# Performance work log

Measured on AMD Instinct MI355X. Metric: run time of the kernel, lower is better.

## Reference

```python
import jax, jax.numpy as jnp
import numpy as np

# tree structure: B trees, layer sizes per tree 2048 -> 256 -> 32 -> 1 (arities 8, 8, 32)
B = 256
N0, N1, N2, N3 = B * 2048, B * 256, B * 32, B * 1
D_IN, HID, OUT = 128, 256, 10
EPS = 1e-5


def _bn(x, g, b):
    # BatchNorm1d, training-mode batch stats (biased variance), as in torch
    mu = jnp.mean(x, axis=0)
    var = jnp.var(x, axis=0)
    return (x - mu) * jax.lax.rsqrt(var + EPS) * g + b


def _tree_layer(pooled, w1, b1, bn1g, bn1b, w2, b2, bng, bnb):
    # MLP(2 layers): Linear -> BN -> ReLU -> Linear, then outer BN -> ReLU (next_layer)
    z = jax.nn.relu(_bn(pooled @ w1 + b1, bn1g, bn1b))
    z = z @ w2 + b2
    return jax.nn.relu(_bn(z, bng, bnb))


def setup_inputs() -> dict:
    key = jax.random.key(0)
    ks = jax.random.split(key, 12)
    s = 0.05
    ar = lambda n: jnp.arange(n, dtype=jnp.int32)
    inp = {
        'x': jax.random.normal(ks[0], (N0, D_IN), jnp.float32),
        # child -> parent index (global, trees are contiguous blocks)
        'parent1': ar(N0) // 8,
        'parent2': ar(N1) // 8,
        'parent3': ar(N2) // 32,
        # node -> tree id per layer (for sum tree-pooling readout)
        'tree0': ar(N0) // 2048,
        'tree1': ar(N1) // 256,
        'tree2': ar(N2) // 32,
        # layer 1 MLP (input_dim -> hidden)
        'l1_w1': jax.random.normal(ks[1], (D_IN, HID), jnp.float32) * s,
        'l1_b1': jnp.zeros((HID,), jnp.float32),
        'l1_bn1g': jnp.ones((HID,), jnp.float32),
        'l1_bn1b': jnp.zeros((HID,), jnp.float32),
        'l1_w2': jax.random.normal(ks[2], (HID, HID), jnp.float32) * s,
        'l1_b2': jnp.zeros((HID,), jnp.float32),
        'l1_bng': jnp.ones((HID,), jnp.float32),
        'l1_bnb': jnp.zeros((HID,), jnp.float32),
        # layers 2 and 3 MLPs (hidden -> hidden), stacked on axis 0
        'lw1': jax.random.normal(ks[3], (2, HID, HID), jnp.float32) * s,
        'lb1': jnp.zeros((2, HID), jnp.float32),
        'lbn1g': jnp.ones((2, HID), jnp.float32),
        'lbn1b': jnp.zeros((2, HID), jnp.float32),
        'lw2': jax.random.normal(ks[4], (2, HID, HID), jnp.float32) * s,
        'lb2': jnp.zeros((2, HID), jnp.float32),
        'lbng': jnp.ones((2, HID), jnp.float32),
        'lbnb': jnp.zeros((2, HID), jnp.float32),
        # prediction heads
        'pred0_w': jax.random.normal(ks[5], (D_IN, OUT), jnp.float32) * s,
        'pred0_b': jnp.zeros((OUT,), jnp.float32),
        'predh_w': jax.random.normal(ks[6], (3, HID, OUT), jnp.float32) * s,
        'predh_b': jnp.zeros((3, OUT), jnp.float32),
    }
    return inp


def reference(x, parent1, parent2, parent3, tree0, tree1, tree2,
              l1_w1, l1_b1, l1_bn1g, l1_bn1b, l1_w2, l1_b2, l1_bng, l1_bnb,
              lw1, lb1, lbn1g, lbn1b, lw2, lb2, lbng, lbnb,
              pred0_w, pred0_b, predh_w, predh_b):
    seg = jax.ops.segment_sum
    h0 = x
    # layer 1: sparse child pooling (spmm == segment_sum) + MLP + BN + ReLU
    h1 = _tree_layer(seg(h0, parent1, num_segments=N1),
                     l1_w1, l1_b1, l1_bn1g, l1_bn1b, l1_w2, l1_b2, l1_bng, l1_bnb)
    h2 = _tree_layer(seg(h1, parent2, num_segments=N2),
                     lw1[0], lb1[0], lbn1g[0], lbn1b[0], lw2[0], lb2[0], lbng[0], lbnb[0])
    h3 = _tree_layer(seg(h2, parent3, num_segments=N3),
                     lw1[1], lb1[1], lbn1g[1], lbn1b[1], lw2[1], lb2[1], lbng[1], lbnb[1])
    # sum tree-pooling readout over layers 0..depth-1, plus root-layer linear
    score = seg(h0, tree0, num_segments=B) @ pred0_w + pred0_b
    score = score + seg(h1, tree1, num_segments=B) @ predh_w[0] + predh_b[0]
    score = score + seg(h2, tree2, num_segments=B) @ predh_w[1] + predh_b[1]
    score = score + h3 @ predh_w[2] + predh_b[2]  # h3 has 1 root per tree -> [B, OUT]
    return score
```

## Files before the change

### kernel.cpp

```cpp
#include <hip/hip_runtime.h>
#include <hip/hip_bf16.h>


#define N0 (256*2048)
#define N1 (256*256)
#define N2 (256*32)
#define NB 256
#define BN_EPS 1e-5f
#define NSLOT 8

typedef __attribute__((ext_vector_type(8))) __bf16 bf16x8;
typedef __attribute__((ext_vector_type(8))) unsigned short u16x8;
typedef __attribute__((ext_vector_type(4))) unsigned short u16x4;
typedef __attribute__((ext_vector_type(4))) float f32x4;

__device__ inline float bf2f(unsigned short b) {
    unsigned u = ((unsigned)b) << 16;
    float f; __builtin_memcpy(&f, &u, 4); return f;
}
__device__ inline unsigned short f2bf(float f) {
    unsigned u; __builtin_memcpy(&u, &f, 4);
    u += 0x7fff + ((u >> 16) & 1);
    return (unsigned short)(u >> 16);
}

__global__ __launch_bounds__(256) void prep_weights(const float* __restrict__ l1_w1,
                                                    const float* __restrict__ l1_w2,
                                                    const float* __restrict__ lw1,
                                                    const float* __restrict__ lw2,
                                                    unsigned short* __restrict__ Wt) {
    int idx = blockIdx.x * 256 + threadIdx.x;
    if (idx >= 360448) return;
    float v;
    if (idx < 32768) {
        int n = idx >> 7, k = idx & 127;
        v = l1_w1[k * 256 + n];
    } else if (idx < 98304) {
        int j = idx - 32768, n = j >> 8, k = j & 255;
        v = l1_w2[k * 256 + n];
    } else if (idx < 163840) {
        int j = idx - 98304, n = j >> 8, k = j & 255;
        v = lw1[k * 256 + n];
    } else if (idx < 229376) {
        int j = idx - 163840, n = j >> 8, k = j & 255;
        v = lw2[k * 256 + n];
    } else if (idx < 294912) {
        int j = idx - 229376, n = j >> 8, k = j & 255;
        v = lw1[65536 + k * 256 + n];
    } else {
        int j = idx - 294912, n = j >> 8, k = j & 255;
        v = lw2[65536 + k * 256 + n];
    }
    Wt[idx] = f2bf(v);
}

__device__ inline void bn_prologue(int tid, const float* __restrict__ partials,
                                   const float* __restrict__ g, const float* __restrict__ b,
                                   float invM, float* sc_lds, float* sh_lds) {
    if (tid < 256) {
        float s = 0.f, s2 = 0.f;
#pragma unroll
        for (int k = 0; k < NSLOT; ++k) {
            s  += partials[k * 512 + tid];
            s2 += partials[k * 512 + 256 + tid];
        }
        float mean = s * invM;
        float var = s2 * invM - mean * mean;
        float sc = g[tid] * rsqrtf(var + BN_EPS);
        sc_lds[tid] = sc;
        sh_lds[tid] = b[tid] - mean * sc;
    }
}

__global__ __launch_bounds__(512) void gemm1_fused(const float* __restrict__ x,
                                                   const unsigned short* __restrict__ Wt,
                                                   const float* __restrict__ bias,
                                                   unsigned short* __restrict__ Z1,
                                                   float* __restrict__ stat_partials,
                                                   float* __restrict__ ts0) {
    constexpr int LDA = 136, LDB = 72;
    __shared__ unsigned short Asb[128 * LDA];
    __shared__ unsigned short Bsb[256 * LDB];
    const int tid = threadIdx.x;
    const int c4 = tid & 31, rg = tid >> 5;
    const int m0 = blockIdx.x * 128;
    const int tree = blockIdx.x >> 1;
    f32x4 colp = {0.f, 0.f, 0.f, 0.f};
#pragma unroll
    for (int i = 0; i < 8; ++i) {
        int row = rg * 8 + i;
        const f32x4* xp = reinterpret_cast<const f32x4*>(x + (size_t)(m0 + row) * 1024 + c4 * 4);
        f32x4 s = {0.f, 0.f, 0.f, 0.f};
#pragma unroll
        for (int c = 0; c < 8; ++c) s += xp[c * 32];
        u16x4 o;
#pragma unroll
        for (int e = 0; e < 4; ++e) o[e] = f2bf(s[e]);
        *reinterpret_cast<u16x4*>(&Asb[row * LDA + c4 * 4]) = o;
        colp += s;
    }
#pragma unroll
    for (int e = 0; e < 4; ++e) atomicAdd(&ts0[tree * 128 + c4 * 4 + e], colp[e]);

    const int wave = tid >> 6, lane = tid & 63;
    const int q = lane >> 4, r = lane & 15;
    const int wc = wave & 3, wr = wave >> 2;
    f32x4 acc[4][4];
#pragma unroll
    for (int i = 0; i < 4; ++i)
#pragma unroll
        for (int j = 0; j < 4; ++j) acc[i][j] = (f32x4){0.f, 0.f, 0.f, 0.f};

#pragma unroll
    for (int s2 = 0; s2 < 2; ++s2) {
#pragma unroll
        for (int i = 0; i < 4; ++i) {
            int v = tid + i * 512;
            int n = v >> 3, kc = v & 7;
            u16x8 d = *reinterpret_cast<const u16x8*>(Wt + (size_t)n * 128 + s2 * 64 + kc * 8);
            *reinterpret_cast<u16x8*>(&Bsb[n * LDB + kc * 8]) = d;
        }
        __syncthreads();
#pragma unroll
        for (int s = 0; s < 2; ++s) {
            bf16x8 a[4], b[4];
#pragma unroll
            for (int i = 0; i < 4; ++i)
                a[i] = *reinterpret_cast<const bf16x8*>(&Asb[(wr * 64 + i * 16 + r) * LDA + s2 * 64 + s * 32 + q * 8]);
#pragma unroll
            for (int j = 0; j < 4; ++j)
                b[j] = *reinterpret_cast<const bf16x8*>(&Bsb[(wc * 64 + j * 16 + r) * LDB + s * 32 + q * 8]);
#pragma unroll
            for (int i = 0; i < 4; ++i)
#pragma unroll
                for (int j = 0; j < 4; ++j)
                    acc[i][j] = __builtin_amdgcn_mfma_f32_16x16x32_bf16(a[i], b[j], acc[i][j], 0, 0, 0);
        }
        __syncthreads();
    }
    float sj[4], s2j[4];
#pragma unroll
    for (int j = 0; j < 4; ++j) {
        float bj = bias[wc * 64 + j * 16 + r];
        float s = 0.f, s2 = 0.f;
#pragma unroll
        for (int i = 0; i < 4; ++i)
#pragma unroll
            for (int e = 0; e < 4; ++e) {
                acc[i][j][e] += bj;
                float v = acc[i][j][e];
                s += v; s2 += v * v;
            }
        s  += __shfl_xor(s, 16);  s  += __shfl_xor(s, 32);
        s2 += __shfl_xor(s2, 16); s2 += __shfl_xor(s2, 32);
        sj[j] = s; s2j[j] = s2;
    }
#pragma unroll
    for (int i = 0; i < 4; ++i)
#pragma unroll
        for (int e = 0; e < 4; ++e) {
            size_t row = m0 + wr * 64 + i * 16 + q * 4 + e;
#pragma unroll
            for (int j = 0; j < 4; ++j)
                Z1[row * 256 + wc * 64 + j * 16 + r] = f2bf(acc[i][j][e]);
        }
    if (q == 0) {
        int slot = blockIdx.x & (NSLOT - 1);
#pragma unroll
        for (int j = 0; j < 4; ++j) {
            int col = wc * 64 + j * 16 + r;
            atomicAdd(&stat_partials[slot * 512 + col], sj[j]);
            atomicAdd(&stat_partials[slot * 512 + 256 + col], s2j[j]);
        }
    }
}

__global__ __launch_bounds__(256) void gemm2_fused(const unsigned short* __restrict__ Z2,
                                                   const float* __restrict__ partials_in,
                                                   const float* __restrict__ bn_g,
                                                   const float* __restrict__ bn_b,
                                                   float invM,
                                                   const unsigned short* __restrict__ Wt2,
                                                   const float* __restrict__ bias,
                                                   unsigned short* __restrict__ Z2a,
                                                   float* __restrict__ stat_partials,
                                                   float* __restrict__ ts1) {
    constexpr int LDA = 264, LDB = 72;
    __shared__ unsigned short Asb[64 * LDA];
    __shared__ unsigned short Bsb[256 * LDB];
    __shared__ float sc_lds[256], sh_lds[256];
    const int tid = threadIdx.x;
    bn_prologue(tid, partials_in, bn_g, bn_b, invM, sc_lds, sh_lds);
    __syncthreads();
    const int c8 = tid & 31, rg = tid >> 5;
    const int m0 = blockIdx.x * 64;
    const int d0 = c8 * 8;
    float sc[8], sh[8], colp[8];
#pragma unroll
    for (int e = 0; e < 8; ++e) { sc[e] = sc_lds[d0 + e]; sh[e] = sh_lds[d0 + e]; colp[e] = 0.f; }
#pragma unroll
    for (int i = 0; i < 8; ++i) {
        int row = rg * 8 + i;
        float s[8];
#pragma unroll
        for (int e = 0; e < 8; ++e) s[e] = 0.f;
#pragma unroll
        for (int c = 0; c < 8; ++c) {
            u16x8 z = *reinterpret_cast<const u16x8*>(Z2 + ((size_t)(m0 + row) * 8 + c) * 256 + d0);
#pragma unroll
            for (int e = 0; e < 8; ++e) {
                float f = sc[e] * bf2f(z[e]) + sh[e];
                s[e] += f > 0.f ? f : 0.f;
            }
        }
        u16x8 o;
#pragma unroll
        for (int e = 0; e < 8; ++e) { o[e] = f2bf(s[e]); colp[e] += s[e]; }
        *reinterpret_cast<u16x8*>(&Asb[row * LDA + d0]) = o;
    }
    {
        int tree = blockIdx.x * 2 + (rg >> 2);
#pragma unroll
        for (int e = 0; e < 8; ++e) atomicAdd(&ts1[tree * 256 + d0 + e], colp[e]);
    }
    const int wave = tid >> 6, lane = tid & 63;
    const int q = lane >> 4, r = lane & 15;
    const int wc = wave;
    f32x4 acc[4][4];
#pragma unroll
    for (int i = 0; i < 4; ++i)
#pragma unroll
        for (int j = 0; j < 4; ++j) acc[i][j] = (f32x4){0.f, 0.f, 0.f, 0.f};

    for (int kt = 0; kt < 4; ++kt) {
#pragma unroll
        for (int i = 0; i < 8; ++i) {
            int v = tid + i * 256;
            int n = v >> 3, kc = v & 7;
            u16x8 d = *reinterpret_cast<const u16x8*>(Wt2 + (size_t)n * 256 + kt * 64 + kc * 8);
            *reinterpret_cast<u16x8*>(&Bsb[n * LDB + kc * 8]) = d;
        }
        __syncthreads();
#pragma unroll
        for (int s = 0; s < 2; ++s) {
            bf16x8 a[4], b[4];
#pragma unroll
            for (int i = 0; i < 4; ++i)
                a[i] = *reinterpret_cast<const bf16x8*>(&Asb[(i * 16 + r) * LDA + kt * 64 + s * 32 + q * 8]);
#pragma unroll
            for (int j = 0; j < 4; ++j)
                b[j] = *reinterpret_cast<const bf16x8*>(&Bsb[(wc * 64 + j * 16 + r) * LDB + s * 32 + q * 8]);
#pragma unroll
            for (int i = 0; i < 4; ++i)
#pragma unroll
                for (int j = 0; j < 4; ++j)
                    acc[i][j] = __builtin_amdgcn_mfma_f32_16x16x32_bf16(a[i], b[j], acc[i][j], 0, 0, 0);
        }
        __syncthreads();
    }
    float sj[4], s2j[4];
#pragma unroll
    for (int j = 0; j < 4; ++j) {
        float bj = bias[wc * 64 + j * 16 + r];
        float s = 0.f, s2 = 0.f;
#pragma unroll
        for (int i = 0; i < 4; ++i)
#pragma unroll
            for (int e = 0; e < 4; ++e) {
                acc[i][j][e] += bj;
                float v = acc[i][j][e];
                s += v; s2 += v * v;
            }
        s  += __shfl_xor(s, 16);  s  += __shfl_xor(s, 32);
        s2 += __shfl_xor(s2, 16); s2 += __shfl_xor(s2, 32);
        sj[j] = s; s2j[j] = s2;
    }
#pragma unroll
    for (int i = 0; i < 4; ++i)
#pragma unroll
        for (int e = 0; e < 4; ++e) {
            size_t row = m0 + i * 16 + q * 4 + e;
#pragma unroll
            for (int j = 0; j < 4; ++j)
                Z2a[row * 256 + wc * 64 + j * 16 + r] = f2bf(acc[i][j][e]);
        }
    if (q == 0) {
        int slot = blockIdx.x & (NSLOT - 1);
#pragma unroll
        for (int j = 0; j < 4; ++j) {
            int col = wc * 64 + j * 16 + r;
            atomicAdd(&stat_partials[slot * 512 + col], sj[j]);
            atomicAdd(&stat_partials[slot * 512 + 256 + col], s2j[j]);
        }
    }
}

template <int KD, bool BN_A, int BM>
__global__ __launch_bounds__(BM * 4) void mfma_gemm(const unsigned short* __restrict__ A,
                                                    const float* __restrict__ partials_in,
                                                    const float* __restrict__ bn_g,
                                                    const float* __restrict__ bn_b,
                                                    float invM,
                                                    const unsigned short* __restrict__ Wt,
                                                    const float* __restrict__ bias,
                                                    unsigned short* __restrict__ C,
                                                    float* __restrict__ stat_partials) {
    constexpr int LDA = 72;
    constexpr int NT = BM * 4;
    __shared__ unsigned short Asb[BM * LDA];
    __shared__ unsigned short Bsb[256 * LDA];
    __shared__ float sc_lds[256], sh_lds[256];
    const int tid = threadIdx.x;
    if (BN_A) {
        bn_prologue(tid, partials_in, bn_g, bn_b, invM, sc_lds, sh_lds);
        __syncthreads();
    }
    const int m0 = blockIdx.x * BM;
    const int wave = tid >> 6, lane = tid & 63;
    const int q = lane >> 4, r = lane & 15;
    const int wc = wave & 3, wr = wave >> 2;

    f32x4 acc[4][4];
#pragma unroll
    for (int i = 0; i < 4; ++i)
#pragma unroll
        for (int j = 0; j < 4; ++j) acc[i][j] = (f32x4){0.f, 0.f, 0.f, 0.f};

    for (int k0 = 0; k0 < KD; k0 += 64) {
#pragma unroll
        for (int i = 0; i < 2; ++i) {
            int v = tid + i * NT;
            int row = v >> 3, kc = v & 7;
            u16x8 d = *reinterpret_cast<const u16x8*>(A + (size_t)(m0 + row) * KD + k0 + kc * 8);
            if (BN_A) {
                u16x8 o;
#pragma unroll
                for (int e = 0; e < 8; ++e) {
                    int k = k0 + kc * 8 + e;
                    float f = sc_lds[k] * bf2f(d[e]) + sh_lds[k];
                    o[e] = f2bf(f > 0.f ? f : 0.f);
                }
                d = o;
            }
            *reinterpret_cast<u16x8*>(&Asb[row * LDA + kc * 8]) = d;
        }
#pragma unroll
        for (int i = 0; i < 2048 / NT; ++i) {
            int v = tid + i * NT;
            int n = v >> 3, kc = v & 7;
            u16x8 d = *reinterpret_cast<const u16x8*>(Wt + (size_t)n * KD + k0 + kc * 8);
            *reinterpret_cast<u16x8*>(&Bsb[n * LDA + kc * 8]) = d;
        }
        __syncthreads();
#pragma unroll
        for (int s = 0; s < 2; ++s) {
            bf16x8 a[4], b[4];
#pragma unroll
            for (int i = 0; i < 4; ++i)
                a[i] = *reinterpret_cast<const bf16x8*>(&Asb[(wr * 64 + i * 16 + r) * LDA + s * 32 + q * 8]);
#pragma unroll
            for (int j = 0; j < 4; ++j)
                b[j] = *reinterpret_cast<const bf16x8*>(&Bsb[(wc * 64 + j * 16 + r) * LDA + s * 32 + q * 8]);
#pragma unroll
            for (int i = 0; i < 4; ++i)
#pragma unroll
                for (int j = 0; j < 4; ++j)
                    acc[i][j] = __builtin_amdgcn_mfma_f32_16x16x32_bf16(a[i], b[j], acc[i][j], 0, 0, 0);
        }
        __syncthreads();
    }
    float sj[4], s2j[4];
#pragma unroll
    for (int j = 0; j < 4; ++j) {
        float bj = bias[wc * 64 + j * 16 + r];
        float s = 0.f, s2 = 0.f;
#pragma unroll
        for (int i = 0; i < 4; ++i)
#pragma unroll
            for (int e = 0; e < 4; ++e) {
                acc[i][j][e] += bj;
                float v = acc[i][j][e];
                s += v; s2 += v * v;
            }
        s  += __shfl_xor(s, 16);  s  += __shfl_xor(s, 32);
        s2 += __shfl_xor(s2, 16); s2 += __shfl_xor(s2, 32);
        sj[j] = s; s2j[j] = s2;
    }
#pragma unroll
    for (int i = 0; i < 4; ++i)
#pragma unroll
        for (int e = 0; e < 4; ++e) {
            size_t row = m0 + wr * 64 + i * 16 + q * 4 + e;
#pragma unroll
            for (int j = 0; j < 4; ++j)
                C[row * 256 + wc * 64 + j * 16 + r] = f2bf(acc[i][j][e]);
        }
    if (q == 0) {
        int slot = blockIdx.x & (NSLOT - 1);
#pragma unroll
        for (int j = 0; j < 4; ++j) {
            int col = wc * 64 + j * 16 + r;
            atomicAdd(&stat_partials[slot * 512 + col], sj[j]);
            atomicAdd(&stat_partials[slot * 512 + 256 + col], s2j[j]);
        }
    }
}

__global__ __launch_bounds__(256) void pool_bn_relu32(const unsigned short* __restrict__ Z,
                                                      const float* __restrict__ partials,
                                                      const float* __restrict__ g,
                                                      const float* __restrict__ b,
                                                      float invM,
                                                      unsigned short* __restrict__ out) {
    __shared__ float sc_lds[256], sh_lds[256];
    int tid = threadIdx.x;
    bn_prologue(tid, partials, g, b, invM, sc_lds, sh_lds);
    __syncthreads();
    int c8 = tid & 31, pl = tid >> 5;
    size_t p = (size_t)blockIdx.x * 8 + pl;
    int d0 = c8 * 8;
    float sc[8], sh[8], s[8];
#pragma unroll
    for (int e = 0; e < 8; ++e) { sc[e] = sc_lds[d0 + e]; sh[e] = sh_lds[d0 + e]; s[e] = 0.f; }
#pragma unroll
    for (int gi = 0; gi < 32; ++gi) {
        u16x8 z = *reinterpret_cast<const u16x8*>(Z + (p * 32 + gi) * 256 + d0);
#pragma unroll
        for (int e = 0; e < 8; ++e) {
            float f = sc[e] * bf2f(z[e]) + sh[e];
            s[e] += f > 0.f ? f : 0.f;
        }
    }
    u16x8 o;
#pragma unroll
    for (int e = 0; e < 8; ++e) o[e] = f2bf(s[e]);
    *reinterpret_cast<u16x8*>(out + p * 256 + d0) = o;
}

__global__ __launch_bounds__(256) void head_kernel(const float* __restrict__ ts0,
                                                   const float* __restrict__ ts1,
                                                   const unsigned short* __restrict__ p3,
                                                   const unsigned short* __restrict__ Z3b,
                                                   const float* __restrict__ partials,
                                                   const float* __restrict__ g,
                                                   const float* __restrict__ b,
                                                   float invM,
                                                   const float* __restrict__ p0w,
                                                   const float* __restrict__ p0b,
                                                   const float* __restrict__ phw,
                                                   const float* __restrict__ phb,
                                                   float* __restrict__ out) {
    __shared__ float sc_lds[256], sh_lds[256];
    int t = blockIdx.x, d = threadIdx.x;
    bn_prologue(d, partials, g, b, invM, sc_lds, sh_lds);
    __syncthreads();
    float acc[10];
#pragma unroll
    for (int o = 0; o < 10; ++o) acc[o] = 0.f;
    if (d < 128) {
        float v = ts0[t * 128 + d];
#pragma unroll
        for (int o = 0; o < 10; ++o) acc[o] += v * p0w[d * 10 + o];
    }
    {
        float v = ts1[t * 256 + d];
#pragma unroll
        for (int o = 0; o < 10; ++o) acc[o] += v * phw[d * 10 + o];
    }
    {
        float v = bf2f(p3[t * 256 + d]);
#pragma unroll
        for (int o = 0; o < 10; ++o) acc[o] += v * phw[2560 + d * 10 + o];
    }
    {
        float v = sc_lds[d] * bf2f(Z3b[t * 256 + d]) + sh_lds[d];
        v = v > 0.f ? v : 0.f;
#pragma unroll
        for (int o = 0; o < 10; ++o) acc[o] += v * phw[5120 + d * 10 + o];
    }
    __shared__ float red[256];
    for (int o = 0; o < 10; ++o) {
        red[d] = acc[o];
        __syncthreads();
        for (int s = 128; s > 0; s >>= 1) {
            if (d < s) red[d] += red[d + s];
            __syncthreads();
        }
        if (d == 0) out[t * 10 + o] = red[0] + p0b[o] + phb[o] + phb[10 + o] + phb[20 + o];
        __syncthreads();
    }
}

extern "C" void kernel_launch(void* const* d_in, const int* in_sizes, int n_in,
                              void* d_out, int out_size, void* d_ws, size_t ws_size,
                              hipStream_t stream) {
    const float* x       = (const float*)d_in[0];
    const float* l1_w1   = (const float*)d_in[7];
    const float* l1_b1   = (const float*)d_in[8];
    const float* l1_bn1g = (const float*)d_in[9];
    const float* l1_bn1b = (const float*)d_in[10];
    const float* l1_w2   = (const float*)d_in[11];
    const float* l1_b2   = (const float*)d_in[12];
    const float* l1_bng  = (const float*)d_in[13];
    const float* l1_bnb  = (const float*)d_in[14];
    const float* lw1     = (const float*)d_in[15];
    const float* lb1     = (const float*)d_in[16];
    const float* lbn1g   = (const float*)d_in[17];
    const float* lbn1b   = (const float*)d_in[18];
    const float* lw2     = (const float*)d_in[19];
    const float* lb2     = (const float*)d_in[20];
    const float* lbng    = (const float*)d_in[21];
    const float* lbnb    = (const float*)d_in[22];
    const float* pred0_w = (const float*)d_in[23];
    const float* pred0_b = (const float*)d_in[24];
    const float* predh_w = (const float*)d_in[25];
    const float* predh_b = (const float*)d_in[26];
    float* out = (float*)d_out;

    uint8_t* wsb = (uint8_t*)d_ws;
    unsigned short* Z1      = (unsigned short*)(wsb + (16ull << 20));
    unsigned short* Z2      = (unsigned short*)(wsb + (48ull << 20));
    unsigned short* Z2a     = (unsigned short*)(wsb + (84ull << 20));
    unsigned short* Z2b     = (unsigned short*)(wsb + (88ull << 20));
    unsigned short* pooled3 = (unsigned short*)(wsb + (92ull << 20));
    unsigned short* Z3a     = (unsigned short*)(wsb + (92ull << 20) + 131072);
    unsigned short* Z3b     = (unsigned short*)(wsb + (92ull << 20) + 262144);
    unsigned short* Wt      = (unsigned short*)(wsb + (93ull << 20));
    float* zbase = (float*)(wsb + (94ull << 20));
    float* ts0   = zbase;
    float* ts1   = zbase + 32768;
    float* stats = zbase + 32768 + 65536;
    auto SP = [&](int i) { return stats + i * (NSLOT * 512); };
    size_t zbytes = (32768 + 65536 + 6 * NSLOT * 512) * sizeof(float);

    hipMemsetAsync(zbase, 0, zbytes, stream);
    prep_weights<<<1408, 256, 0, stream>>>(l1_w1, l1_w2, lw1, lw2, Wt);

    gemm1_fused<<<N1 / 128, 512, 0, stream>>>(x, Wt, l1_b1, Z1, SP(0), ts0);
    mfma_gemm<256, true, 128><<<N1 / 128, 512, 0, stream>>>(
        Z1, SP(0), l1_bn1g, l1_bn1b, 1.f / N1, Wt + 32768, l1_b2, Z2, SP(1));

    gemm2_fused<<<N2 / 64, 256, 0, stream>>>(
        Z2, SP(1), l1_bng, l1_bnb, 1.f / N1, Wt + 98304, lb1, Z2a, SP(2), ts1);
    mfma_gemm<256, true, 64><<<N2 / 64, 256, 0, stream>>>(
        Z2a, SP(2), lbn1g, lbn1b, 1.f / N2, Wt + 163840, lb2, Z2b, SP(3));
    pool_bn_relu32<<<NB / 8, 256, 0, stream>>>(Z2b, SP(3), lbng, lbnb, 1.f / N2, pooled3);

    mfma_gemm<256, false, 64><<<NB / 64, 256, 0, stream>>>(
        pooled3, nullptr, nullptr, nullptr, 0.f, Wt + 229376, lb1 + 256, Z3a, SP(4));
    mfma_gemm<256, true, 64><<<NB / 64, 256, 0, stream>>>(
        Z3a, SP(4), lbn1g + 256, lbn1b + 256, 1.f / NB, Wt + 294912, lb2 + 256, Z3b, SP(5));

    head_kernel<<<NB, 256, 0, stream>>>(ts0, ts1, pooled3, Z3b, SP(5),
                                        lbng + 256, lbnb + 256, 1.f / NB,
                                        pred0_w, pred0_b, predh_w, predh_b, out);
}
```

Measured before the change: 191.4 us.

## Retile layer-2 GEMMs to 32-row blocks and fuse layer-3 into one kernel

Layer-2 GEMMs now use 32-row tiles with 512 threads, which doubles the block count from 128 to 256 so more CUs are busy, and the tree-sum readout is reduced in LDS instead of with atomics. The two tiny layer-3 GEMMs and their BN stats are fused into a single-block kernel that computes the BN scale and shift itself, removing kernel launches and the stat-partial round trips. The trade-off is that the single-block layer-3 kernel runs serially on one CU, and the B weights are reloaded per 32-row block.

```diff
diff --git a/kernel.cpp b/kernel.cpp
--- a/kernel.cpp
+++ b/kernel.cpp
@@ -54,9 +54,9 @@
     Wt[idx] = f2bf(v);
 }
 
-__device__ inline void bn_prologue(int tid, const float* __restrict__ partials,
-                                   const float* __restrict__ g, const float* __restrict__ b,
-                                   float invM, float* sc_lds, float* sh_lds) {
+__device__ __forceinline__ void bn_prologue(int tid, const float* __restrict__ partials,
+                                            const float* __restrict__ g, const float* __restrict__ b,
+                                            float invM, float* sc_lds, float* sh_lds) {
     if (tid < 256) {
         float s = 0.f, s2 = 0.f;
 #pragma unroll
@@ -163,126 +163,6 @@
 #pragma unroll
             for (int j = 0; j < 4; ++j)
                 Z1[row * 256 + wc * 64 + j * 16 + r] = f2bf(acc[i][j][e]);
-        }
-    if (q == 0) {
-        int slot = blockIdx.x & (NSLOT - 1);
-#pragma unroll
-        for (int j = 0; j < 4; ++j) {
-            int col = wc * 64 + j * 16 + r;
-            atomicAdd(&stat_partials[slot * 512 + col], sj[j]);
-            atomicAdd(&stat_partials[slot * 512 + 256 + col], s2j[j]);
-        }
-    }
-}
-
-__global__ __launch_bounds__(256) void gemm2_fused(const unsigned short* __restrict__ Z2,
-                                                   const float* __restrict__ partials_in,
-                                                   const float* __restrict__ bn_g,
-                                                   const float* __restrict__ bn_b,
-                                                   float invM,
-                                                   const unsigned short* __restrict__ Wt2,
-                                                   const float* __restrict__ bias,
-                                                   unsigned short* __restrict__ Z2a,
-                                                   float* __restrict__ stat_partials,
-                                                   float* __restrict__ ts1) {
-    constexpr int LDA = 264, LDB = 72;
-    __shared__ unsigned short Asb[64 * LDA];
-    __shared__ unsigned short Bsb[256 * LDB];
-    __shared__ float sc_lds[256], sh_lds[256];
-    const int tid = threadIdx.x;
-    bn_prologue(tid, partials_in, bn_g, bn_b, invM, sc_lds, sh_lds);
-    __syncthreads();
-    const int c8 = tid & 31, rg = tid >> 5;
-    const int m0 = blockIdx.x * 64;
-    const int d0 = c8 * 8;
-    float sc[8], sh[8], colp[8];
-#pragma unroll
-    for (int e = 0; e < 8; ++e) { sc[e] = sc_lds[d0 + e]; sh[e] = sh_lds[d0 + e]; colp[e] = 0.f; }
-#pragma unroll
-    for (int i = 0; i < 8; ++i) {
-        int row = rg * 8 + i;
-        float s[8];
-#pragma unroll
-        for (int e = 0; e < 8; ++e) s[e] = 0.f;
-#pragma unroll
-        for (int c = 0; c < 8; ++c) {
-            u16x8 z = *reinterpret_cast<const u16x8*>(Z2 + ((size_t)(m0 + row) * 8 + c) * 256 + d0);
-#pragma unroll
-            for (int e = 0; e < 8; ++e) {
-                float f = sc[e] * bf2f(z[e]) + sh[e];
-                s[e] += f > 0.f ? f : 0.f;
-            }
-        }
-        u16x8 o;
-#pragma unroll
-        for (int e = 0; e < 8; ++e) { o[e] = f2bf(s[e]); colp[e] += s[e]; }
-        *reinterpret_cast<u16x8*>(&Asb[row * LDA + d0]) = o;
-    }
-    {
-        int tree = blockIdx.x * 2 + (rg >> 2);
-#pragma unroll
-        for (int e = 0; e < 8; ++e) atomicAdd(&ts1[tree * 256 + d0 + e], colp[e]);
-    }
-    const int wave = tid >> 6, lane = tid & 63;
-    const int q = lane >> 4, r = lane & 15;
-    const int wc = wave;
-    f32x4 acc[4][4];
-#pragma unroll
-    for (int i = 0; i < 4; ++i)
-#pragma unroll
-        for (int j = 0; j < 4; ++j) acc[i][j] = (f32x4){0.f, 0.f, 0.f, 0.f};
-
-    for (int kt = 0; kt < 4; ++kt) {
-#pragma unroll
-        for (int i = 0; i < 8; ++i) {
-            int v = tid + i * 256;
-            int n = v >> 3, kc = v & 7;
-            u16x8 d = *reinterpret_cast<const u16x8*>(Wt2 + (size_t)n * 256 + kt * 64 + kc * 8);
-            *reinterpret_cast<u16x8*>(&Bsb[n * LDB + kc * 8]) = d;
-        }
-        __syncthreads();
-#pragma unroll
-        for (int s = 0; s < 2; ++s) {
-            bf16x8 a[4], b[4];
-#pragma unroll
-            for (int i = 0; i < 4; ++i)
-                a[i] = *reinterpret_cast<const bf16x8*>(&Asb[(i * 16 + r) * LDA + kt * 64 + s * 32 + q * 8]);
-#pragma unroll
-            for (int j = 0; j < 4; ++j)
-                b[j] = *reinterpret_cast<const bf16x8*>(&Bsb[(wc * 64 + j * 16 + r) * LDB + s * 32 + q * 8]);
-#pragma unroll
-            for (int i = 0; i < 4; ++i)
-#pragma unroll
-                for (int j = 0; j < 4; ++j)
-                    acc[i][j] = __builtin_amdgcn_mfma_f32_16x16x32_bf16(a[i], b[j], acc[i][j], 0, 0, 0);
-        }
-        __syncthreads();
-    }
-    float sj[4], s2j[4];
-#pragma unroll
-    for (int j = 0; j < 4; ++j) {
-        float bj = bias[wc * 64 + j * 16 + r];
-        float s = 0.f, s2 = 0.f;
-#pragma unroll
-        for (int i = 0; i < 4; ++i)
-#pragma unroll
-            for (int e = 0; e < 4; ++e) {
-                acc[i][j][e] += bj;
-                float v = acc[i][j][e];
-                s += v; s2 += v * v;
-            }
-        s  += __shfl_xor(s, 16);  s  += __shfl_xor(s, 32);
-        s2 += __shfl_xor(s2, 16); s2 += __shfl_xor(s2, 32);
-        sj[j] = s; s2j[j] = s2;
-    }
-#pragma unroll
-    for (int i = 0; i < 4; ++i)
-#pragma unroll
-        for (int e = 0; e < 4; ++e) {
-            size_t row = m0 + i * 16 + q * 4 + e;
-#pragma unroll
-            for (int j = 0; j < 4; ++j)
-                Z2a[row * 256 + wc * 64 + j * 16 + r] = f2bf(acc[i][j][e]);
         }
     if (q == 0) {
         int slot = blockIdx.x & (NSLOT - 1);
@@ -406,15 +286,165 @@
     }
 }
 
+__device__ __forceinline__ void gemm32_kloop(const unsigned short* __restrict__ Wt,
+                                             const float* __restrict__ bias,
+                                             unsigned short* __restrict__ C,
+                                             float* __restrict__ statsOut,
+                                             int m0, int slot,
+                                             const unsigned short* Asb, unsigned short* Bsb) {
+    const int tid = threadIdx.x, wave = tid >> 6, lane = tid & 63;
+    const int q = lane >> 4, r = lane & 15;
+    const int wc = wave & 3, wr = wave >> 2;
+    f32x4 acc[4];
+#pragma unroll
+    for (int j = 0; j < 4; ++j) acc[j] = (f32x4){0.f, 0.f, 0.f, 0.f};
+    for (int kt = 0; kt < 4; ++kt) {
+#pragma unroll
+        for (int i = 0; i < 4; ++i) {
+            int v = tid + i * 512;
+            int n = v >> 3, kc = v & 7;
+            *reinterpret_cast<u16x8*>(&Bsb[n * 72 + kc * 8]) =
+                *reinterpret_cast<const u16x8*>(Wt + (size_t)n * 256 + kt * 64 + kc * 8);
+        }
+        __syncthreads();
+#pragma unroll
+        for (int s = 0; s < 2; ++s) {
+            bf16x8 a = *reinterpret_cast<const bf16x8*>(&Asb[(wr * 16 + r) * 264 + kt * 64 + s * 32 + q * 8]);
+#pragma unroll
+            for (int j = 0; j < 4; ++j) {
+                bf16x8 b = *reinterpret_cast<const bf16x8*>(&Bsb[(wc * 64 + j * 16 + r) * 72 + s * 32 + q * 8]);
+                acc[j] = __builtin_amdgcn_mfma_f32_16x16x32_bf16(a, b, acc[j], 0, 0, 0);
+            }
+        }
+        __syncthreads();
+    }
+#pragma unroll
+    for (int j = 0; j < 4; ++j) {
+        float bj = bias[wc * 64 + j * 16 + r];
+        float s = 0.f, s2 = 0.f;
+#pragma unroll
+        for (int e = 0; e < 4; ++e) {
+            acc[j][e] += bj;
+            float v = acc[j][e];
+            s += v; s2 += v * v;
+        }
+        s  += __shfl_xor(s, 16);  s  += __shfl_xor(s, 32);
+        s2 += __shfl_xor(s2, 16); s2 += __shfl_xor(s2, 32);
+#pragma unroll
+        for (int e = 0; e < 4; ++e)
+            C[(size_t)(m0 + wr * 16 + q * 4 + e) * 256 + wc * 64 + j * 16 + r] = f2bf(acc[j][e]);
+        if (q == 0) {
+            int col = wc * 64 + j * 16 + r;
+            atomicAdd(&statsOut[slot * 512 + col], s);
+            atomicAdd(&statsOut[slot * 512 + 256 + col], s2);
+        }
+    }
+}
+
+__device__ __forceinline__ void stage_A32(const unsigned short* __restrict__ A, int m0,
+                                          bool bn, const float* sc_lds, const float* sh_lds,
+                                          unsigned short* Asb) {
+    const int tid = threadIdx.x;
+#pragma unroll
+    for (int i = 0; i < 2; ++i) {
+        int v = tid + i * 512;
+        int row = v >> 5, kc = v & 31;
+        u16x8 d = *reinterpret_cast<const u16x8*>(A + (size_t)(m0 + row) * 256 + kc * 8);
+        if (bn) {
+            u16x8 o;
+#pragma unroll
+            for (int e = 0; e < 8; ++e) {
+                int k = kc * 8 + e;
+                float f = sc_lds[k] * bf2f(d[e]) + sh_lds[k];
+                o[e] = f2bf(f > 0.f ? f : 0.f);
+            }
+            d = o;
+        }
+        *reinterpret_cast<u16x8*>(&Asb[row * 264 + kc * 8]) = d;
+    }
+}
+
+__global__ __launch_bounds__(512) void gemm2a_kernel(const unsigned short* __restrict__ Z2,
+                                                     const float* __restrict__ partials_in,
+                                                     const float* __restrict__ g,
+                                                     const float* __restrict__ b,
+                                                     const unsigned short* __restrict__ Wt2,
+                                                     const float* __restrict__ bias,
+                                                     unsigned short* __restrict__ Z2a,
+                                                     float* __restrict__ statsOut,
+                                                     float* __restrict__ ts1) {
+    __shared__ unsigned short Asb[32 * 264];
+    __shared__ unsigned short Bsb[256 * 72];
+    __shared__ float scsh[512];
+    const int tid = threadIdx.x, bid = blockIdx.x;
+    bn_prologue(tid, partials_in, g, b, 1.f / N1, scsh, scsh + 256);
+    __syncthreads();
+    const int c8 = tid & 31, rg = tid >> 5;
+    const int m0 = bid * 32, d0 = c8 * 8;
+    float sc[8], sh[8], colp[8];
+#pragma unroll
+    for (int e = 0; e < 8; ++e) { sc[e] = scsh[d0 + e]; sh[e] = scsh[256 + d0 + e]; colp[e] = 0.f; }
+#pragma unroll
+    for (int i = 0; i < 2; ++i) {
+        int row = rg * 2 + i;
+        float s[8];
+#pragma unroll
+        for (int e = 0; e < 8; ++e) s[e] = 0.f;
+#pragma unroll
+        for (int c = 0; c < 8; ++c) {
+            u16x8 z = *reinterpret_cast<const u16x8*>(Z2 + ((size_t)(m0 + row) * 8 + c) * 256 + d0);
+#pragma unroll
+            for (int e = 0; e < 8; ++e) {
+                float f = sc[e] * bf2f(z[e]) + sh[e];
+                s[e] += f > 0.f ? f : 0.f;
+            }
+        }
+        u16x8 o;
+#pragma unroll
+        for (int e = 0; e < 8; ++e) { o[e] = f2bf(s[e]); colp[e] += s[e]; }
+        *reinterpret_cast<u16x8*>(&Asb[row * 264 + d0]) = o;
+    }
+    float* red = (float*)Bsb;
+#pragma unroll
+    for (int e = 0; e < 8; ++e) red[rg * 256 + d0 + e] = colp[e];
+    __syncthreads();
+    if (tid < 256) {
+        float t = 0.f;
+#pragma unroll
+        for (int gi = 0; gi < 16; ++gi) t += red[gi * 256 + tid];
+        ts1[bid * 256 + tid] = t;
+    }
+    __syncthreads();
+    gemm32_kloop(Wt2, bias, Z2a, statsOut, m0, bid & (NSLOT - 1), Asb, Bsb);
+}
+
+__global__ __launch_bounds__(512) void gemm2b_kernel(const unsigned short* __restrict__ Z2a,
+                                                     const float* __restrict__ partials_in,
+                                                     const float* __restrict__ g,
+                                                     const float* __restrict__ b,
+                                                     const unsigned short* __restrict__ Wt2,
+                                                     const float* __restrict__ bias,
+                                                     unsigned short* __restrict__ Z2b,
+                                                     float* __restrict__ statsOut) {
+    __shared__ unsigned short Asb[32 * 264];
+    __shared__ unsigned short Bsb[256 * 72];
+    __shared__ float scsh[512];
+    const int tid = threadIdx.x, bid = blockIdx.x;
+    bn_prologue(tid, partials_in, g, b, 1.f / N2, scsh, scsh + 256);
+    __syncthreads();
+    stage_A32(Z2a, bid * 32, true, scsh, scsh + 256, Asb);
+    __syncthreads();
+    gemm32_kloop(Wt2, bias, Z2b, statsOut, bid * 32, bid & (NSLOT - 1), Asb, Bsb);
+}
+
 __global__ __launch_bounds__(256) void pool_bn_relu32(const unsigned short* __restrict__ Z,
                                                       const float* __restrict__ partials,
                                                       const float* __restrict__ g,
                                                       const float* __restrict__ b,
-                                                      float invM,
                                                       unsigned short* __restrict__ out) {
     __shared__ float sc_lds[256], sh_lds[256];
     int tid = threadIdx.x;
-    bn_prologue(tid, partials, g, b, invM, sc_lds, sh_lds);
+    bn_prologue(tid, partials, g, b, 1.f / N2, sc_lds, sh_lds);
     __syncthreads();
     int c8 = tid & 31, pl = tid >> 5;
     size_t p = (size_t)blockIdx.x * 8 + pl;
@@ -437,22 +467,146 @@
     *reinterpret_cast<u16x8*>(out + p * 256 + d0) = o;
 }
 
+__global__ __launch_bounds__(512) void layer3_kernel(const unsigned short* __restrict__ pooled3,
+                                                     const unsigned short* __restrict__ Wt3a,
+                                                     const unsigned short* __restrict__ Wt3b,
+                                                     const float* __restrict__ b3a,
+                                                     const float* __restrict__ b3b,
+                                                     const float* __restrict__ g4,
+                                                     const float* __restrict__ b4,
+                                                     const float* __restrict__ g5,
+                                                     const float* __restrict__ b5,
+                                                     unsigned short* __restrict__ Z3a,
+                                                     unsigned short* __restrict__ Z3b,
+                                                     float* __restrict__ ss5) {
+    __shared__ unsigned short Asb[64 * 264];
+    __shared__ unsigned short Bsb[256 * 72];
+    __shared__ float colsum[256], colsq[256], scsh[512];
+    const int tid = threadIdx.x, wave = tid >> 6, lane = tid & 63;
+    const int q = lane >> 4, r = lane & 15;
+    const int wr = wave >> 2, wc = wave & 3;
+    if (tid < 256) { colsum[tid] = 0.f; colsq[tid] = 0.f; }
+    __syncthreads();
+
+#pragma unroll 1
+    for (int phase = 0; phase < 2; ++phase) {
+        const unsigned short* Ain = phase ? Z3a : pooled3;
+        const unsigned short* Wp  = phase ? Wt3b : Wt3a;
+        const float* bp           = phase ? b3b : b3a;
+        unsigned short* Cout      = phase ? Z3b : Z3a;
+#pragma unroll 1
+        for (int mt = 0; mt < 4; ++mt) {
+            const int m0 = mt * 64;
+#pragma unroll
+            for (int i = 0; i < 4; ++i) {
+                int v = tid + i * 512;
+                int row = v >> 5, kc = v & 31;
+                u16x8 d = *reinterpret_cast<const u16x8*>(Ain + (size_t)(m0 + row) * 256 + kc * 8);
+                if (phase) {
+                    u16x8 o;
+#pragma unroll
+                    for (int e = 0; e < 8; ++e) {
+                        int k = kc * 8 + e;
+                        float f = scsh[k] * bf2f(d[e]) + scsh[256 + k];
+                        o[e] = f2bf(f > 0.f ? f : 0.f);
+                    }
+                    d = o;
+                }
+                *reinterpret_cast<u16x8*>(&Asb[row * 264 + kc * 8]) = d;
+            }
+            f32x4 acc[2][4];
+#pragma unroll
+            for (int i = 0; i < 2; ++i)
+#pragma unroll
+                for (int j = 0; j < 4; ++j) acc[i][j] = (f32x4){0.f, 0.f, 0.f, 0.f};
+            for (int kt = 0; kt < 4; ++kt) {
+#pragma unroll
+                for (int i = 0; i < 4; ++i) {
+                    int v = tid + i * 512;
+                    int n = v >> 3, kc = v & 7;
+                    *reinterpret_cast<u16x8*>(&Bsb[n * 72 + kc * 8]) =
+                        *reinterpret_cast<const u16x8*>(Wp + (size_t)n * 256 + kt * 64 + kc * 8);
+                }
+                __syncthreads();
+#pragma unroll
+                for (int s = 0; s < 2; ++s) {
+                    bf16x8 a[2], b[4];
+#pragma unroll
+                    for (int i = 0; i < 2; ++i)
+                        a[i] = *reinterpret_cast<const bf16x8*>(&Asb[(wr * 32 + i * 16 + r) * 264 + kt * 64 + s * 32 + q * 8]);
+#pragma unroll
+                    for (int j = 0; j < 4; ++j)
+                        b[j] = *reinterpret_cast<const bf16x8*>(&Bsb[(wc * 64 + j * 16 + r) * 72 + s * 32 + q * 8]);
+#pragma unroll
+                    for (int i = 0; i < 2; ++i)
+#pragma unroll
+                        for (int j = 0; j < 4; ++j)
+                            acc[i][j] = __builtin_amdgcn_mfma_f32_16x16x32_bf16(a[i], b[j], acc[i][j], 0, 0, 0);
+                }
+                __syncthreads();
+            }
+#pragma unroll
+            for (int j = 0; j < 4; ++j) {
+                float bj = bp[wc * 64 + j * 16 + r];
+                float s = 0.f, s2 = 0.f;
+#pragma unroll
+                for (int i = 0; i < 2; ++i)
+#pragma unroll
+                    for (int e = 0; e < 4; ++e) {
+                        acc[i][j][e] += bj;
+                        float v = acc[i][j][e];
+                        s += v; s2 += v * v;
+                    }
+                s  += __shfl_xor(s, 16);  s  += __shfl_xor(s, 32);
+                s2 += __shfl_xor(s2, 16); s2 += __shfl_xor(s2, 32);
+#pragma unroll
+                for (int i = 0; i < 2; ++i)
+#pragma unroll
+                    for (int e = 0; e < 4; ++e)
+                        Cout[(size_t)(m0 + wr * 32 + i * 16 + q * 4 + e) * 256 + wc * 64 + j * 16 + r] =
+                            f2bf(acc[i][j][e]);
+                if (q == 0) {
+                    int col = wc * 64 + j * 16 + r;
+                    atomicAdd(&colsum[col], s);
+                    atomicAdd(&colsq[col], s2);
+                }
+            }
+            __syncthreads();
+        }
+        __syncthreads();
+        if (tid < 256) {
+            float mean = colsum[tid] * (1.f / NB);
+            float var = colsq[tid] * (1.f / NB) - mean * mean;
+            const float* gg = phase ? g5 : g4;
+            const float* bb = phase ? b5 : b4;
+            float sc = gg[tid] * rsqrtf(var + BN_EPS);
+            if (phase) {
+                ss5[tid] = sc;
+                ss5[256 + tid] = bb[tid] - mean * sc;
+            } else {
+                scsh[tid] = sc;
+                scsh[256 + tid] = bb[tid] - mean * sc;
+            }
+            colsum[tid] = 0.f; colsq[tid] = 0.f;
+        }
+        __syncthreads();
+    }
+}
+
 __global__ __launch_bounds__(256) void head_kernel(const float* __restrict__ ts0,
                                                    const float* __restrict__ ts1,
                                                    const unsigned short* __restrict__ p3,
                                                    const unsigned short* __restrict__ Z3b,
-                                                   const float* __restrict__ partials,
-                                                   const float* __restrict__ g,
-                                                   const float* __restrict__ b,
-                                                   float invM,
+                                                   const float* __restrict__ ss5,
                                                    const float* __restrict__ p0w,
                                                    const float* __restrict__ p0b,
                                                    const float* __restrict__ phw,
                                                    const float* __restrict__ phb,
                                                    float* __restrict__ out) {
-    __shared__ float sc_lds[256], sh_lds[256];
+    __shared__ float scsh[512];
     int t = blockIdx.x, d = threadIdx.x;
-    bn_prologue(d, partials, g, b, invM, sc_lds, sh_lds);
+    scsh[d] = ss5[d];
+    scsh[256 + d] = ss5[256 + d];
     __syncthreads();
     float acc[10];
 #pragma unroll
@@ -473,7 +627,7 @@
         for (int o = 0; o < 10; ++o) acc[o] += v * phw[2560 + d * 10 + o];
     }
     {
-        float v = sc_lds[d] * bf2f(Z3b[t * 256 + d]) + sh_lds[d];
+        float v = scsh[d] * bf2f(Z3b[t * 256 + d]) + scsh[256 + d];
         v = v > 0.f ? v : 0.f;
 #pragma unroll
         for (int o = 0; o < 10; ++o) acc[o] += v * phw[5120 + d * 10 + o];
@@ -530,6 +684,7 @@
     float* ts0   = zbase;
     float* ts1   = zbase + 32768;
     float* stats = zbase + 32768 + 65536;
+    float* ss5   = stats + 6 * NSLOT * 512;
     auto SP = [&](int i) { return stats + i * (NSLOT * 512); };
     size_t zbytes = (32768 + 65536 + 6 * NSLOT * 512) * sizeof(float);
 
@@ -540,18 +695,18 @@
     mfma_gemm<256, true, 128><<<N1 / 128, 512, 0, stream>>>(
         Z1, SP(0), l1_bn1g, l1_bn1b, 1.f / N1, Wt + 32768, l1_b2, Z2, SP(1));
 
-    gemm2_fused<<<N2 / 64, 256, 0, stream>>>(
-        Z2, SP(1), l1_bng, l1_bnb, 1.f / N1, Wt + 98304, lb1, Z2a, SP(2), ts1);
-    mfma_gemm<256, true, 64><<<N2 / 64, 256, 0, stream>>>(
-        Z2a, SP(2), lbn1g, lbn1b, 1.f / N2, Wt + 163840, lb2, Z2b, SP(3));
-    pool_bn_relu32<<<NB / 8, 256, 0, stream>>>(Z2b, SP(3), lbng, lbnb, 1.f / N2, pooled3);
-
-    mfma_gemm<256, false, 64><<<NB / 64, 256, 0, stream>>>(
-        pooled3, nullptr, nullptr, nullptr, 0.f, Wt + 229376, lb1 + 256, Z3a, SP(4));
-    mfma_gemm<256, true, 64><<<NB / 64, 256, 0, stream>>>(
-        Z3a, SP(4), lbn1g + 256, lbn1b + 256, 1.f / NB, Wt + 294912, lb2 + 256, Z3b, SP(5));
-
-    head_kernel<<<NB, 256, 0, stream>>>(ts0, ts1, pooled3, Z3b, SP(5),
-                                        lbng + 256, lbnb + 256, 1.f / NB,
+    gemm2a_kernel<<<N2 / 32, 512, 0, stream>>>(
+        Z2, SP(1), l1_bng, l1_bnb, Wt + 98304, lb1, Z2a, SP(2), ts1);
+    gemm2b_kernel<<<N2 / 32, 512, 0, stream>>>(
+        Z2a, SP(2), lbn1g, lbn1b, Wt + 163840, lb2, Z2b, SP(3));
+    pool_bn_relu32<<<NB / 8, 256, 0, stream>>>(Z2b, SP(3), lbng, lbnb, pooled3);
+
+    layer3_kernel<<<1, 512, 0, stream>>>(pooled3, Wt + 229376, Wt + 294912,
+                                         lb1 + 256, lb2 + 256,
+                                         lbn1g + 256, lbn1b + 256,
+                                         lbng + 256, lbnb + 256,
+                                         Z3a, Z3b, ss5);
+
+    head_kernel<<<NB, 256, 0, stream>>>(ts0, ts1, pooled3, Z3b, ss5,
                                         pred0_w, pred0_b, predh_w, predh_b, out);
 }
```

Result: slower. 200.1 us (+4.5%).
